# Optimization experiments

Hardware: AMD Instinct MI355X
Metric: run time of the kernel (lower is better)

## Reference

```python
import jax, jax.numpy as jnp
import numpy as np

B, C, H, W = 2, 512, 64, 64
NUM_GROUPS = 32
EPS = 1e-6


def setup_inputs() -> dict:
    key = jax.random.key(0)
    ks = jax.random.split(key, 6)
    s = 1.0 / np.sqrt(C)
    return {
        "x": jax.random.normal(ks[0], (B, C, H, W), dtype=jnp.float32),
        "gn_scale": jnp.ones((C,), jnp.float32),
        "gn_bias": jnp.zeros((C,), jnp.float32),
        "wq": jax.random.normal(ks[1], (C, C), jnp.float32) * s,
        "bq": jnp.zeros((C,), jnp.float32),
        "wk": jax.random.normal(ks[2], (C, C), jnp.float32) * s,
        "bk": jnp.zeros((C,), jnp.float32),
        "wv": jax.random.normal(ks[3], (C, C), jnp.float32) * s,
        "bv": jnp.zeros((C,), jnp.float32),
        "wp": jax.random.normal(ks[4], (C, C), jnp.float32) * s,
        "bp": jnp.zeros((C,), jnp.float32),
    }


def group_norm(x, scale, bias):
    # x: [b, c, h, w]; GroupNorm with NUM_GROUPS groups, eps=1e-6, affine
    b, c, h, w = x.shape
    xg = x.reshape(b, NUM_GROUPS, c // NUM_GROUPS, h, w)
    mean = jnp.mean(xg, axis=(2, 3, 4), keepdims=True)
    var = jnp.var(xg, axis=(2, 3, 4), keepdims=True)
    xg = (xg - mean) * jax.lax.rsqrt(var + EPS)
    xn = xg.reshape(b, c, h, w)
    return xn * scale[None, :, None, None] + bias[None, :, None, None]


def reference(x, gn_scale, gn_bias, wq, bq, wk, bk, wv, bv, wp, bp):
    b, c, h, w = x.shape
    n = h * w
    hn = group_norm(x, gn_scale, gn_bias).reshape(b, c, n)  # [b,c,n]
    # 1x1 convs == per-pixel linear over channels
    q = jnp.einsum('dc,bcn->bdn', wq, hn) + bq[None, :, None]
    k = jnp.einsum('dc,bcn->bdn', wk, hn) + bk[None, :, None]
    v = jnp.einsum('dc,bcn->bdn', wv, hn) + bv[None, :, None]
    # attn[b,i,j] = softmax_j( q[:, :, i] . k[:, :, j] / sqrt(c) )
    attn = jnp.einsum('bci,bcj->bij', q, k) * (float(c) ** -0.5)
    attn = jax.nn.softmax(attn, axis=-1)
    out = jnp.einsum('bcj,bij->bci', v, attn)  # [b,c,n]
    out = jnp.einsum('dc,bcn->bdn', wp, out) + bp[None, :, None]
    return x + out.reshape(b, c, h, w)
```

## Files before the change

### kernel.cpp

```cpp
#include <hip/hip_runtime.h>

typedef __bf16 bf16x8 __attribute__((ext_vector_type(8)));
typedef float f32x4 __attribute__((ext_vector_type(4)));
typedef int i32x8 __attribute__((ext_vector_type(8)));
typedef _Float16 h8 __attribute__((ext_vector_type(8)));


#if defined(__has_builtin)
#if __has_builtin(__builtin_amdgcn_global_load_lds)
#define HAS_GLL 1
#endif
#endif

__device__ __forceinline__ void async_copy16(const void* g, void* l) {
#ifdef HAS_GLL
    __builtin_amdgcn_global_load_lds(
        (const __attribute__((address_space(1))) unsigned int*)g,
        (__attribute__((address_space(3))) unsigned int*)l, 16, 0, 0);
#else
    *(int4*)l = *(const int4*)g;
#endif
}

__device__ __forceinline__ unsigned char to_fp8(float v) {
    return (unsigned char)(__builtin_amdgcn_cvt_pk_fp8_f32(v, v, 0, false) & 0xFF);
}

#define MXSCALE 0x7F7F7F7F

__global__ __launch_bounds__(256) void prep_kernel(
    const float* __restrict__ x, float* __restrict__ ps,
    const float* __restrict__ wq, const float* __restrict__ wk,
    const float* __restrict__ wv, const float* __restrict__ wp,
    const float* __restrict__ bq, const float* __restrict__ bk,
    unsigned char* __restrict__ wqk8, unsigned char* __restrict__ wv8,
    __bf16* __restrict__ wp_b, float* __restrict__ bqk) {
    if (blockIdx.x >= 1024) {
        int idx = (blockIdx.x - 1024) * 256 + threadIdx.x;
        wqk8[idx] = to_fp8(wq[idx]);
        wqk8[262144 + idx] = to_fp8(wk[idx]);
        wv8[idx] = to_fp8(wv[idx]);
        wp_b[idx] = (__bf16)wp[idx];
        if (idx < 512) {
            bqk[idx] = bq[idx];
            bqk[512 + idx] = bk[idx];
        }
        return;
    }
    int blk = blockIdx.x;
    const float4* base = (const float4*)x + (size_t)blk * 1024;
    float s1 = 0.f, s2 = 0.f;
#pragma unroll
    for (int i = 0; i < 4; ++i) {
        float4 v = base[threadIdx.x + (i << 8)];
        s1 += v.x + v.y + v.z + v.w;
        s2 += v.x * v.x + v.y * v.y + v.z * v.z + v.w * v.w;
    }
    for (int off = 32; off >= 1; off >>= 1) {
        s1 += __shfl_xor(s1, off);
        s2 += __shfl_xor(s2, off);
    }
    __shared__ float r1[4], r2[4];
    int wave = threadIdx.x >> 6, lane = threadIdx.x & 63;
    if (lane == 0) { r1[wave] = s1; r2[wave] = s2; }
    __syncthreads();
    if (threadIdx.x == 0) {
        ps[blk] = r1[0] + r1[1] + r1[2] + r1[3];
        ps[1024 + blk] = r2[0] + r2[1] + r2[2] + r2[3];
    }
}

__global__ __launch_bounds__(256) void gn_apply_kernel(const float* __restrict__ x,
                                                       const float* __restrict__ gn_scale,
                                                       const float* __restrict__ gn_bias,
                                                       const float* __restrict__ ps,
                                                       unsigned char* __restrict__ hn8) {
    __shared__ float tile[32][33];
    int b = blockIdx.z;
    int n0 = blockIdx.x * 32, c0 = blockIdx.y * 32;
    int tx = threadIdx.x & 31, ty = threadIdx.x >> 5;
    const float* xb = x + (size_t)b * 512 * 4096;
#pragma unroll
    for (int r = 0; r < 4; ++r) {
        int c = ty + r * 8;
        tile[c][tx] = xb[(size_t)(c0 + c) * 4096 + n0 + tx];
    }
    int c = c0 + tx;
    int g = (b << 5) + (c >> 4);
    float s1 = 0.f, s2 = 0.f;
#pragma unroll
    for (int i = 0; i < 16; ++i) {
        s1 += ps[(g << 4) + i];
        s2 += ps[1024 + (g << 4) + i];
    }
    float m = s1 * (1.f / 65536.f);
    float var = s2 * (1.f / 65536.f) - m * m;
    float rs = rsqrtf(var + 1e-6f);
    float sc = gn_scale[c] * rs;
    float bi = gn_bias[c] - m * sc;
    __syncthreads();
    unsigned char* outp = hn8 + (size_t)b * 4096 * 512;
#pragma unroll
    for (int r = 0; r < 4; ++r) {
        int n = ty + r * 8;
        float v = tile[tx][n];
        outp[(size_t)(n0 + n) * 512 + c] = to_fp8(v * sc + bi);
    }
}

template <int BN, int OUT_MODE, int BIAS_MODE>
__global__ __launch_bounds__(256) void mx_gemm_kernel(
    const unsigned char* __restrict__ A, int lda, long bsA,
    const unsigned char* __restrict__ Bt, int ldb, long bsB,
    void* __restrict__ C, int ldc, long bsC,
    const float* __restrict__ bias, int K, float scale) {
    constexpr int NT = BN / 32;
    __shared__ __align__(16) unsigned char As[128 * 128];
    __shared__ __align__(16) unsigned char Bs[BN * 128];
    const int tid = threadIdx.x;
    const int lane = tid & 63, wave = tid >> 6;
    const int ln = lane & 15, q = lane >> 4;
    const int wm = (wave >> 1) << 6;
    const int wn = (wave & 1) * (BN / 2);
    const int b = blockIdx.z;
    const long m0 = (long)blockIdx.y * 128, n0 = (long)blockIdx.x * BN;
    const unsigned char* Ab = A + (long)b * bsA + m0 * lda;
    const unsigned char* Bb = Bt + (long)b * bsB + n0 * ldb;

    f32x4 acc[4][NT] = {};

    for (int k0 = 0; k0 < K; k0 += 128) {
        __syncthreads();
#pragma unroll
        for (int p = 0; p < 4; ++p) {
            int c = (p << 8) + tid;
            int row = c >> 3, sg = (c & 7) << 4;
            async_copy16(Ab + (long)row * lda + k0 + sg, &As[c << 4]);
        }
#pragma unroll
        for (int p = 0; p < BN / 32; ++p) {
            int c = (p << 8) + tid;
            int row = c >> 3, sg = (c & 7) << 4;
            async_copy16(Bb + (long)row * ldb + k0 + sg, &Bs[c << 4]);
        }
        __syncthreads();
        i32x8 af[4], bf[NT];
#pragma unroll
        for (int t = 0; t < 4; ++t) {
            const unsigned char* ap = &As[(wm + t * 16 + ln) * 128 + (q << 5)];
            *(int4*)&af[t] = *(const int4*)ap;
            *((int4*)&af[t] + 1) = *(const int4*)(ap + 16);
        }
#pragma unroll
        for (int t = 0; t < NT; ++t) {
            const unsigned char* bp = &Bs[(wn + t * 16 + ln) * 128 + (q << 5)];
            *(int4*)&bf[t] = *(const int4*)bp;
            *((int4*)&bf[t] + 1) = *(const int4*)(bp + 16);
        }
#pragma unroll
        for (int mt = 0; mt < 4; ++mt)
#pragma unroll
            for (int nt = 0; nt < NT; ++nt)
                acc[mt][nt] = __builtin_amdgcn_mfma_scale_f32_16x16x128_f8f6f4(
                    af[mt], bf[nt], acc[mt][nt], 0, 0, 0, MXSCALE, 0, MXSCALE);
    }

#pragma unroll
    for (int mt = 0; mt < 4; ++mt) {
#pragma unroll
        for (int nt = 0; nt < NT; ++nt) {
            long col = n0 + wn + nt * 16 + ln;
#pragma unroll
            for (int r = 0; r < 4; ++r) {
                long row = m0 + wm + mt * 16 + (q << 2) + r;
                float v = acc[mt][nt][r] * scale;
                if (BIAS_MODE == 1) v += bias[row];
                if (BIAS_MODE == 2) v += bias[col];
                long off = (long)b * bsC + row * (long)ldc + col;
                if (OUT_MODE == 0) {
                    ((unsigned char*)C)[off] = to_fp8(v);
                } else {
                    ((_Float16*)C)[off] = (_Float16)v;
                }
            }
        }
    }
}

__global__ __launch_bounds__(256) void softmax_kernel(_Float16* __restrict__ S) {
    long row = blockIdx.x;
    _Float16* srow = S + (row << 12);
    int tid = threadIdx.x;
    h8 a = ((const h8*)srow)[tid];
    h8 c = ((const h8*)srow)[tid + 256];
    float v[16];
#pragma unroll
    for (int p = 0; p < 8; ++p) {
        v[p] = (float)a[p];
        v[8 + p] = (float)c[p];
    }
    float mx = -1e30f;
#pragma unroll
    for (int p = 0; p < 16; ++p) mx = fmaxf(mx, v[p]);
    for (int off = 32; off >= 1; off >>= 1) mx = fmaxf(mx, __shfl_xor(mx, off));
    __shared__ float red[4], red2[4];
    int wave = tid >> 6, lane = tid & 63;
    if (lane == 0) red[wave] = mx;
    __syncthreads();
    mx = fmaxf(fmaxf(red[0], red[1]), fmaxf(red[2], red[3]));
    float s = 0.f;
#pragma unroll
    for (int p = 0; p < 16; ++p) {
        v[p] = __expf(v[p] - mx);
        s += v[p];
    }
    for (int off = 32; off >= 1; off >>= 1) s += __shfl_xor(s, off);
    if (lane == 0) red2[wave] = s;
    __syncthreads();
    s = red2[0] + red2[1] + red2[2] + red2[3];
    float inv64 = 64.f / s;
    int w[4];
#pragma unroll
    for (int i = 0; i < 4; ++i) {
        w[i] = __builtin_amdgcn_cvt_pk_fp8_f32(v[4 * i] * inv64, v[4 * i + 1] * inv64, 0, false);
        w[i] = __builtin_amdgcn_cvt_pk_fp8_f32(v[4 * i + 2] * inv64, v[4 * i + 3] * inv64, w[i], true);
    }
    ((int2*)srow)[tid] = make_int2(w[0], w[1]);
    ((int2*)srow)[tid + 256] = make_int2(w[2], w[3]);
}

__global__ __launch_bounds__(256) void mx_pv_kernel(const unsigned char* __restrict__ P,
                                                    const unsigned char* __restrict__ V,
                                                    __bf16* __restrict__ O) {
    __shared__ __align__(16) unsigned char As[128 * 128];
    __shared__ __align__(16) unsigned char Bs[64 * 128];
    const int tid = threadIdx.x;
    const int lane = tid & 63, wave = tid >> 6;
    const int ln = lane & 15, q = lane >> 4;
    const int wm = (wave >> 1) << 6, wn = (wave & 1) << 5;
    const int b = blockIdx.x >> 5;
    const long m0 = (long)(blockIdx.x & 31) * 128;
    const long n0 = (long)blockIdx.y * 64;
    const unsigned char* Pb = P + ((long)b * 4096 + m0) * 8192;
    const unsigned char* Vb = V + ((long)b * 512 + n0) * 4096;

    f32x4 acc[4][2] = {};

    for (int k0 = 0; k0 < 4096; k0 += 128) {
        __syncthreads();
#pragma unroll
        for (int p = 0; p < 4; ++p) {
            int c = (p << 8) + tid;
            int row = c >> 3, sg = (c & 7) << 4;
            async_copy16(Pb + (long)row * 8192 + k0 + sg, &As[c << 4]);
        }
#pragma unroll
        for (int p = 0; p < 2; ++p) {
            int c = (p << 8) + tid;
            int row = c >> 3, sg = (c & 7) << 4;
            async_copy16(Vb + (long)row * 4096 + k0 + sg, &Bs[c << 4]);
        }
        __syncthreads();
        i32x8 af[4], bf[2];
#pragma unroll
        for (int t = 0; t < 4; ++t) {
            const unsigned char* ap = &As[(wm + t * 16 + ln) * 128 + (q << 5)];
            *(int4*)&af[t] = *(const int4*)ap;
            *((int4*)&af[t] + 1) = *(const int4*)(ap + 16);
        }
#pragma unroll
        for (int t = 0; t < 2; ++t) {
            const unsigned char* bp = &Bs[(wn + t * 16 + ln) * 128 + (q << 5)];
            *(int4*)&bf[t] = *(const int4*)bp;
            *((int4*)&bf[t] + 1) = *(const int4*)(bp + 16);
        }
#pragma unroll
        for (int mt = 0; mt < 4; ++mt)
#pragma unroll
            for (int nt = 0; nt < 2; ++nt)
                acc[mt][nt] = __builtin_amdgcn_mfma_scale_f32_16x16x128_f8f6f4(
                    af[mt], bf[nt], acc[mt][nt], 0, 0, 0, MXSCALE, 0, MXSCALE);
    }

    __bf16* Ob = O + (long)b * 4096 * 512;
#pragma unroll
    for (int mt = 0; mt < 4; ++mt) {
#pragma unroll
        for (int nt = 0; nt < 2; ++nt) {
            long col = n0 + wn + nt * 16 + ln;
#pragma unroll
            for (int r = 0; r < 4; ++r) {
                long row = m0 + wm + mt * 16 + (q << 2) + r;
                Ob[row * 512 + col] = (__bf16)(acc[mt][nt][r] * 0.015625f);
            }
        }
    }
}

__global__ __launch_bounds__(256) void proj_kernel(
    const __bf16* __restrict__ A, const __bf16* __restrict__ Bt, long bsB,
    float* __restrict__ C, long bsC, const float* __restrict__ bias,
    const float* __restrict__ resid) {
    __shared__ __align__(16) __bf16 As[128][64];
    __shared__ __align__(16) __bf16 Bs[64][64];
    const int tid = threadIdx.x;
    const int wave = tid >> 6, lane = tid & 63;
    const int q = lane >> 4, ln = lane & 15;
    const int wm = wave << 5;
    const long m0 = (long)blockIdx.y * 128, n0 = (long)blockIdx.x * 64;
    const int b = blockIdx.z;
    const __bf16* Ab = A + m0 * 512;
    const __bf16* Bb = Bt + (long)b * bsB + n0 * 512;

    f32x4 acc[2][4] = {};

    for (int k0 = 0; k0 < 512; k0 += 64) {
        __syncthreads();
#pragma unroll
        for (int p = 0; p < 4; ++p) {
            int c = (p << 8) + tid;
            int row = c >> 3, sg = (c & 7) << 3;
            async_copy16(Ab + (long)row * 512 + k0 + sg, &As[0][0] + (c << 3));
        }
#pragma unroll
        for (int p = 0; p < 2; ++p) {
            int c = (p << 8) + tid;
            int row = c >> 3, sg = (c & 7) << 3;
            async_copy16(Bb + (long)row * 512 + k0 + sg, &Bs[0][0] + (c << 3));
        }
        __syncthreads();
#pragma unroll
        for (int kk = 0; kk < 2; ++kk) {
            bf16x8 af[2], bfr[4];
#pragma unroll
            for (int mt = 0; mt < 2; ++mt)
                af[mt] = *(const bf16x8*)(&As[wm + mt * 16 + ln][(kk << 5) + (q << 3)]);
#pragma unroll
            for (int nt = 0; nt < 4; ++nt)
                bfr[nt] = *(const bf16x8*)(&Bs[nt * 16 + ln][(kk << 5) + (q << 3)]);
#pragma unroll
            for (int mt = 0; mt < 2; ++mt)
#pragma unroll
                for (int nt = 0; nt < 4; ++nt)
                    acc[mt][nt] = __builtin_amdgcn_mfma_f32_16x16x32_bf16(
                        af[mt], bfr[nt], acc[mt][nt], 0, 0, 0);
        }
    }

#pragma unroll
    for (int mt = 0; mt < 2; ++mt) {
#pragma unroll
        for (int nt = 0; nt < 4; ++nt) {
            long col = n0 + nt * 16 + ln;
#pragma unroll
            for (int r = 0; r < 4; ++r) {
                long row = m0 + wm + mt * 16 + (q << 2) + r;
                long off = (long)b * bsC + row * 4096 + col;
                C[off] = acc[mt][nt][r] + bias[row] + resid[off];
            }
        }
    }
}

extern "C" void kernel_launch(void* const* d_in, const int* in_sizes, int n_in,
                              void* d_out, int out_size, void* d_ws, size_t ws_size,
                              hipStream_t stream) {
    const float* x = (const float*)d_in[0];
    const float* gn_scale = (const float*)d_in[1];
    const float* gn_bias = (const float*)d_in[2];
    const float* wq = (const float*)d_in[3];
    const float* bq = (const float*)d_in[4];
    const float* wk = (const float*)d_in[5];
    const float* bk = (const float*)d_in[6];
    const float* wv = (const float*)d_in[7];
    const float* bv = (const float*)d_in[8];
    const float* wp = (const float*)d_in[9];
    const float* bp = (const float*)d_in[10];
    float* out = (float*)d_out;

    char* ws = (char*)d_ws;
    unsigned char* wqk8 = (unsigned char*)(ws + 0x0);
    unsigned char* wv8 = (unsigned char*)(ws + 0x80000);
    __bf16* wp_b = (__bf16*)(ws + 0xC0000);
    float* bqk = (float*)(ws + 0x140000);
    float* psum = (float*)(ws + 0x142000);
    unsigned char* hn8 = (unsigned char*)(ws + 0x150000);
    unsigned char* qk8 = (unsigned char*)(ws + 0x550000);
    unsigned char* v8 = (unsigned char*)(ws + 0xD50000);
    __bf16* o_t = (__bf16*)(ws + 0x1150000);
    _Float16* Sbuf = (_Float16*)(ws + 0x1950000);
    (void)ws_size;

    prep_kernel<<<2048, 256, 0, stream>>>(x, psum, wq, wk, wv, wp, bq, bk,
                                          wqk8, wv8, wp_b, bqk);
    gn_apply_kernel<<<dim3(128, 16, 2), 256, 0, stream>>>(x, gn_scale, gn_bias,
                                                          psum, hn8);

    mx_gemm_kernel<128, 0, 2><<<dim3(8, 32, 2), 256, 0, stream>>>(
        hn8, 512, 4096l * 512, wqk8, 512, 0,
        qk8, 1024, 4096l * 1024, bqk, 512, 1.f);

    mx_gemm_kernel<64, 0, 1><<<dim3(64, 4, 2), 256, 0, stream>>>(
        wv8, 512, 0, hn8, 512, 4096l * 512,
        v8, 4096, 512l * 4096, bv, 512, 1.f);

    const float attn_scale = 0.044194173824159216f;
    mx_gemm_kernel<128, 1, 0><<<dim3(32, 32, 2), 256, 0, stream>>>(
        qk8, 1024, 4096l * 1024, qk8 + 512, 1024, 4096l * 1024,
        Sbuf, 4096, 4096l * 4096, nullptr, 512, attn_scale);
    softmax_kernel<<<8192, 256, 0, stream>>>(Sbuf);
    mx_pv_kernel<<<dim3(64, 8), 256, 0, stream>>>(
        (const unsigned char*)Sbuf, v8, o_t);

    proj_kernel<<<dim3(64, 4, 2), 256, 0, stream>>>(
        wp_b, o_t, 4096l * 512, out, 512l * 4096, bp, x);
}
```

Before: 201.0 us.

## Store attention scores as fp8, merge QKV GEMMs, deepen PV k-tile

The S=QK^T GEMM now writes scores in fp8 instead of fp16, halving S buffer traffic, and softmax reads fp8 and writes its fp8 probabilities in place with a compact row stride. The Q/K and V projection GEMMs are merged into one launch with a z-dispatch to cut launch overhead and fill the machine better. The PV kernel now loads 256-wide k-tiles, halving the number of barriers per output tile. Storing pre-softmax logits in fp8 loses precision in the scores and risks accuracy. The larger PV tiles raise LDS use and may lower occupancy.

```diff
diff --git a/kernel.cpp b/kernel.cpp
--- a/kernel.cpp
+++ b/kernel.cpp
@@ -3,7 +3,6 @@
 typedef __bf16 bf16x8 __attribute__((ext_vector_type(8)));
 typedef float f32x4 __attribute__((ext_vector_type(4)));
 typedef int i32x8 __attribute__((ext_vector_type(8)));
-typedef _Float16 h8 __attribute__((ext_vector_type(8)));
 
 
 #if defined(__has_builtin)
@@ -109,23 +108,18 @@
 }
 
 template <int BN, int OUT_MODE, int BIAS_MODE>
-__global__ __launch_bounds__(256) void mx_gemm_kernel(
-    const unsigned char* __restrict__ A, int lda, long bsA,
-    const unsigned char* __restrict__ Bt, int ldb, long bsB,
-    void* __restrict__ C, int ldc, long bsC,
-    const float* __restrict__ bias, int K, float scale) {
+__device__ __forceinline__ void mx_gemm_body(
+    const unsigned char* __restrict__ Ab, int lda,
+    const unsigned char* __restrict__ Bb, int ldb,
+    void* __restrict__ C, int ldc,
+    const float* __restrict__ bias, int K, float scale,
+    long m0, long n0, unsigned char* As, unsigned char* Bs) {
     constexpr int NT = BN / 32;
-    __shared__ __align__(16) unsigned char As[128 * 128];
-    __shared__ __align__(16) unsigned char Bs[BN * 128];
     const int tid = threadIdx.x;
     const int lane = tid & 63, wave = tid >> 6;
     const int ln = lane & 15, q = lane >> 4;
     const int wm = (wave >> 1) << 6;
     const int wn = (wave & 1) * (BN / 2);
-    const int b = blockIdx.z;
-    const long m0 = (long)blockIdx.y * 128, n0 = (long)blockIdx.x * BN;
-    const unsigned char* Ab = A + (long)b * bsA + m0 * lda;
-    const unsigned char* Bb = Bt + (long)b * bsB + n0 * ldb;
 
     f32x4 acc[4][NT] = {};
 
@@ -176,7 +170,7 @@
                 float v = acc[mt][nt][r] * scale;
                 if (BIAS_MODE == 1) v += bias[row];
                 if (BIAS_MODE == 2) v += bias[col];
-                long off = (long)b * bsC + row * (long)ldc + col;
+                long off = row * (long)ldc + col;
                 if (OUT_MODE == 0) {
                     ((unsigned char*)C)[off] = to_fp8(v);
                 } else {
@@ -187,18 +181,61 @@
     }
 }
 
-__global__ __launch_bounds__(256) void softmax_kernel(_Float16* __restrict__ S) {
+__global__ __launch_bounds__(256) void qkv_kernel(
+    const unsigned char* __restrict__ hn8, const unsigned char* __restrict__ wqk8,
+    const unsigned char* __restrict__ wv8, const float* __restrict__ bqk,
+    const float* __restrict__ bv, unsigned char* __restrict__ qk8,
+    unsigned char* __restrict__ v8) {
+    __shared__ __align__(16) unsigned char As[128 * 128];
+    __shared__ __align__(16) unsigned char Bs[128 * 128];
+    int z = blockIdx.z;
+    if (z < 2) {
+        long b = z;
+        long m0 = (long)blockIdx.y * 128, n0 = (long)blockIdx.x * 128;
+        mx_gemm_body<128, 0, 2>(hn8 + b * 4096 * 512 + m0 * 512, 512,
+                                wqk8 + n0 * 512, 512,
+                                qk8 + b * 4096 * 1024, 1024,
+                                bqk, 512, 1.f, m0, n0, As, Bs);
+    } else {
+        long b = z - 2;
+        int flat = blockIdx.y * 8 + blockIdx.x;
+        long m0 = (long)(flat >> 6) * 128, n0 = (long)(flat & 63) * 64;
+        mx_gemm_body<64, 0, 1>(wv8 + m0 * 512, 512,
+                               hn8 + b * 4096 * 512 + n0 * 512, 512,
+                               v8 + b * 512 * 4096, 4096,
+                               bv, 512, 1.f, m0, n0, As, Bs);
+    }
+}
+
+__global__ __launch_bounds__(256) void mx_s_kernel(const unsigned char* __restrict__ QK,
+                                                   unsigned char* __restrict__ S,
+                                                   float scale) {
+    __shared__ __align__(16) unsigned char As[128 * 128];
+    __shared__ __align__(16) unsigned char Bs[128 * 128];
+    long b = blockIdx.z;
+    long m0 = (long)blockIdx.y * 128, n0 = (long)blockIdx.x * 128;
+    mx_gemm_body<128, 0, 0>(QK + b * 4096 * 1024 + m0 * 1024, 1024,
+                            QK + b * 4096 * 1024 + n0 * 1024 + 512, 1024,
+                            S + b * 4096 * 4096, 4096,
+                            nullptr, 512, scale, m0, n0, As, Bs);
+}
+
+#define CVT4(dst, base, word)                                   \
+    dst[base + 0] = __builtin_amdgcn_cvt_f32_fp8(word, 0);      \
+    dst[base + 1] = __builtin_amdgcn_cvt_f32_fp8(word, 1);      \
+    dst[base + 2] = __builtin_amdgcn_cvt_f32_fp8(word, 2);      \
+    dst[base + 3] = __builtin_amdgcn_cvt_f32_fp8(word, 3);
+
+__global__ __launch_bounds__(256) void softmax_kernel(unsigned char* __restrict__ S) {
     long row = blockIdx.x;
-    _Float16* srow = S + (row << 12);
+    unsigned char* srow = S + (row << 12);
     int tid = threadIdx.x;
-    h8 a = ((const h8*)srow)[tid];
-    h8 c = ((const h8*)srow)[tid + 256];
+    int4 d = ((const int4*)srow)[tid];
     float v[16];
-#pragma unroll
-    for (int p = 0; p < 8; ++p) {
-        v[p] = (float)a[p];
-        v[8 + p] = (float)c[p];
-    }
+    CVT4(v, 0, d.x)
+    CVT4(v, 4, d.y)
+    CVT4(v, 8, d.z)
+    CVT4(v, 12, d.w)
     float mx = -1e30f;
 #pragma unroll
     for (int p = 0; p < 16; ++p) mx = fmaxf(mx, v[p]);
@@ -225,15 +262,14 @@
         w[i] = __builtin_amdgcn_cvt_pk_fp8_f32(v[4 * i] * inv64, v[4 * i + 1] * inv64, 0, false);
         w[i] = __builtin_amdgcn_cvt_pk_fp8_f32(v[4 * i + 2] * inv64, v[4 * i + 3] * inv64, w[i], true);
     }
-    ((int2*)srow)[tid] = make_int2(w[0], w[1]);
-    ((int2*)srow)[tid + 256] = make_int2(w[2], w[3]);
+    ((int4*)srow)[tid] = make_int4(w[0], w[1], w[2], w[3]);
 }
 
 __global__ __launch_bounds__(256) void mx_pv_kernel(const unsigned char* __restrict__ P,
                                                     const unsigned char* __restrict__ V,
                                                     __bf16* __restrict__ O) {
-    __shared__ __align__(16) unsigned char As[128 * 128];
-    __shared__ __align__(16) unsigned char Bs[64 * 128];
+    __shared__ __align__(16) unsigned char As[128 * 256];
+    __shared__ __align__(16) unsigned char Bs[64 * 256];
     const int tid = threadIdx.x;
     const int lane = tid & 63, wave = tid >> 6;
     const int ln = lane & 15, q = lane >> 4;
@@ -241,45 +277,50 @@
     const int b = blockIdx.x >> 5;
     const long m0 = (long)(blockIdx.x & 31) * 128;
     const long n0 = (long)blockIdx.y * 64;
-    const unsigned char* Pb = P + ((long)b * 4096 + m0) * 8192;
+    const unsigned char* Pb = P + ((long)b * 4096 + m0) * 4096;
     const unsigned char* Vb = V + ((long)b * 512 + n0) * 4096;
 
     f32x4 acc[4][2] = {};
 
-    for (int k0 = 0; k0 < 4096; k0 += 128) {
-        __syncthreads();
+    for (int k0 = 0; k0 < 4096; k0 += 256) {
+        __syncthreads();
+#pragma unroll
+        for (int p = 0; p < 8; ++p) {
+            int c = (p << 8) + tid;
+            int row = c >> 4, sg = (c & 15) << 4;
+            async_copy16(Pb + (long)row * 4096 + k0 + sg, &As[c << 4]);
+        }
 #pragma unroll
         for (int p = 0; p < 4; ++p) {
             int c = (p << 8) + tid;
-            int row = c >> 3, sg = (c & 7) << 4;
-            async_copy16(Pb + (long)row * 8192 + k0 + sg, &As[c << 4]);
-        }
-#pragma unroll
-        for (int p = 0; p < 2; ++p) {
-            int c = (p << 8) + tid;
-            int row = c >> 3, sg = (c & 7) << 4;
+            int row = c >> 4, sg = (c & 15) << 4;
             async_copy16(Vb + (long)row * 4096 + k0 + sg, &Bs[c << 4]);
         }
         __syncthreads();
-        i32x8 af[4], bf[2];
-#pragma unroll
-        for (int t = 0; t < 4; ++t) {
-            const unsigned char* ap = &As[(wm + t * 16 + ln) * 128 + (q << 5)];
-            *(int4*)&af[t] = *(const int4*)ap;
-            *((int4*)&af[t] + 1) = *(const int4*)(ap + 16);
-        }
-#pragma unroll
-        for (int t = 0; t < 2; ++t) {
-            const unsigned char* bp = &Bs[(wn + t * 16 + ln) * 128 + (q << 5)];
-            *(int4*)&bf[t] = *(const int4*)bp;
-            *((int4*)&bf[t] + 1) = *(const int4*)(bp + 16);
-        }
-#pragma unroll
-        for (int mt = 0; mt < 4; ++mt)
-#pragma unroll
-            for (int nt = 0; nt < 2; ++nt)
-                acc[mt][nt] = __builtin_amdgcn_mfma_scale_f32_16x16x128_f8f6f4(
-                    af[mt], bf[nt], acc[mt][nt], 0, 0, 0, MXSCALE, 0, MXSCALE);
+#pragma unroll
+        for (int kk = 0; kk < 2; ++kk) {
+            i32x8 af[4], bf[2];
+#pragma unroll
+            for (int t = 0; t < 4; ++t) {
+                const unsigned char* ap =
+                    &As[(wm + t * 16 + ln) * 256 + (kk << 7) + (q << 5)];
+                *(int4*)&af[t] = *(const int4*)ap;
+                *((int4*)&af[t] + 1) = *(const int4*)(ap + 16);
+            }
+#pragma unroll
+            for (int t = 0; t < 2; ++t) {
+                const unsigned char* bp =
+                    &Bs[(wn + t * 16 + ln) * 256 + (kk << 7) + (q << 5)];
+                *(int4*)&bf[t] = *(const int4*)bp;
+                *((int4*)&bf[t] + 1) = *(const int4*)(bp + 16);
+            }
+#pragma unroll
+            for (int mt = 0; mt < 4; ++mt)
+#pragma unroll
+                for (int nt = 0; nt < 2; ++nt)
+                    acc[mt][nt] = __builtin_amdgcn_mfma_scale_f32_16x16x128_f8f6f4(
+                        af[mt], bf[nt], acc[mt][nt], 0, 0, 0, MXSCALE, 0, MXSCALE);
+        }
     }
 
     __bf16* Ob = O + (long)b * 4096 * 512;
@@ -388,7 +429,7 @@
     unsigned char* qk8 = (unsigned char*)(ws + 0x550000);
     unsigned char* v8 = (unsigned char*)(ws + 0xD50000);
     __bf16* o_t = (__bf16*)(ws + 0x1150000);
-    _Float16* Sbuf = (_Float16*)(ws + 0x1950000);
+    unsigned char* S8 = (unsigned char*)(ws + 0x1950000);
     (void)ws_size;
 
     prep_kernel<<<2048, 256, 0, stream>>>(x, psum, wq, wk, wv, wp, bq, bk,
@@ -396,21 +437,13 @@
     gn_apply_kernel<<<dim3(128, 16, 2), 256, 0, stream>>>(x, gn_scale, gn_bias,
                                                           psum, hn8);
 
-    mx_gemm_kernel<128, 0, 2><<<dim3(8, 32, 2), 256, 0, stream>>>(
-        hn8, 512, 4096l * 512, wqk8, 512, 0,
-        qk8, 1024, 4096l * 1024, bqk, 512, 1.f);
-
-    mx_gemm_kernel<64, 0, 1><<<dim3(64, 4, 2), 256, 0, stream>>>(
-        wv8, 512, 0, hn8, 512, 4096l * 512,
-        v8, 4096, 512l * 4096, bv, 512, 1.f);
+    qkv_kernel<<<dim3(8, 32, 4), 256, 0, stream>>>(hn8, wqk8, wv8, bqk, bv,
+                                                   qk8, v8);
 
     const float attn_scale = 0.044194173824159216f;
-    mx_gemm_kernel<128, 1, 0><<<dim3(32, 32, 2), 256, 0, stream>>>(
-        qk8, 1024, 4096l * 1024, qk8 + 512, 1024, 4096l * 1024,
-        Sbuf, 4096, 4096l * 4096, nullptr, 512, attn_scale);
-    softmax_kernel<<<8192, 256, 0, stream>>>(Sbuf);
-    mx_pv_kernel<<<dim3(64, 8), 256, 0, stream>>>(
-        (const unsigned char*)Sbuf, v8, o_t);
+    mx_s_kernel<<<dim3(32, 32, 2), 256, 0, stream>>>(qk8, S8, attn_scale);
+    softmax_kernel<<<8192, 256, 0, stream>>>(S8);
+    mx_pv_kernel<<<dim3(64, 8), 256, 0, stream>>>(S8, v8, o_t);
 
     proj_kernel<<<dim3(64, 4, 2), 256, 0, stream>>>(
         wp_b, o_t, 4096l * 512, out, 512l * 4096, bp, x);
```

Measured after the change: 214.6 us. 1.07x slower.
